# Kernel tuning notes

Measured on AMD Instinct MI355X. Metric: run time of the kernel, lower is better.

Reference implementation:

```python
import jax, jax.numpy as jnp
import numpy as np

HIDDEN = 1024   # config.hidden_dim
FF = 4096       # expert MLP hidden (4*hidden)
E = 8           # config.num_experts
K = 2           # config.num_selected_experts (top_k)


def setup_inputs() -> dict:
    key = jax.random.key(0)
    ks = jax.random.split(key, 5)
    s = 0.02
    x = jax.random.normal(ks[0], (2, 2048, HIDDEN), jnp.float32)
    Wr = jax.random.normal(ks[1], (HIDDEN, E), jnp.float32) * s   # router (no bias)
    W1 = jax.random.normal(ks[2], (E, HIDDEN, FF), jnp.float32) * s
    b1 = jnp.zeros((E, FF), jnp.float32)
    W2 = jax.random.normal(ks[3], (E, FF, HIDDEN), jnp.float32) * s
    b2 = jnp.zeros((E, HIDDEN), jnp.float32)
    return {"x": x, "Wr": Wr, "W1": W1, "b1": b1, "W2": W2, "b2": b2}


def reference(x, Wr, W1, b1, W2, b2):
    xs = x.reshape(-1, x.shape[-1])            # [T, H]
    router_logits = xs @ Wr                    # [T, E]
    # softmax_order == 'softmax_topk': softmax over all experts in fp32, then top-k
    all_probs = jax.nn.softmax(router_logits.astype(jnp.float32), axis=-1)
    weights, selected_experts = jax.lax.top_k(all_probs, K)   # [T, K], [T, K]
    T = xs.shape[0]
    # per-token per-expert combine weight (zero where expert not selected)
    combine = jnp.zeros((T, E), jnp.float32).at[
        jnp.arange(T)[:, None], selected_experts
    ].add(weights)                              # [T, E]
    out = jnp.zeros_like(xs)
    for e in range(E):                          # fixed small loop over experts
        h = jax.nn.gelu(xs @ W1[e] + b1[e])     # [T, FF]
        y = h @ W2[e] + b2[e]                   # [T, H]
        out = out + combine[:, e, None].astype(xs.dtype) * y
    return out.reshape(x.shape), router_logits, selected_experts
```

## Files before the change

kernel.cpp:

```cpp
#include <hip/hip_runtime.h>
#include <hip/hip_bf16.h>
#include <stdint.h>

#define HID 1024
#define FFD 4096
#define FFH 2048
#define NE  8
#define NTOK 4096
#define BM 128
#define BN 128
#define BK 32
#define RBCAP 72
#define ROWCAP (RBCAP*BM)

typedef __attribute__((ext_vector_type(8))) short short8;
typedef __attribute__((ext_vector_type(4))) float f32x4;

__device__ __forceinline__ unsigned short f2bf(float f){
  union { float f; unsigned u; } v; v.f = f;
  return (unsigned short)((v.u + 0x7FFFu + ((v.u >> 16) & 1u)) >> 16);
}

__device__ __forceinline__ float gelu_f(float x){
  float u = 0.7978845608028654f * (x + 0.044715f * x * x * x);
  return 0.5f * x * (1.0f + tanhf(u));
}

__device__ __forceinline__ void gload_lds16(const void* g, void* l){
  __builtin_amdgcn_global_load_lds((const __attribute__((address_space(1))) void*)g,
                                   (__attribute__((address_space(3))) void*)l,
                                   16, 0, 0);
}

__global__ __launch_bounds__(256) void router_k(
    const float* __restrict__ x, const float* __restrict__ Wr,
    float* __restrict__ out_logits, float* __restrict__ out_sel,
    int* __restrict__ tok_sel, float* __restrict__ tok_w)
{
  const int lane = threadIdx.x & 63;
  const int t = (blockIdx.x << 2) + (threadIdx.x >> 6);
  const float* xr = x + (size_t)t * HID;
  double acc[NE];
  #pragma unroll
  for (int e = 0; e < NE; ++e) acc[e] = 0.0;
  #pragma unroll
  for (int i = 0; i < 4; ++i) {
    const int h0 = i * 256 + lane * 4;
    float4 xv = *(const float4*)(xr + h0);
    #pragma unroll
    for (int r = 0; r < 4; ++r) {
      float xs = (&xv.x)[r];
      float4 w0 = *(const float4*)(Wr + (size_t)(h0 + r) * NE);
      float4 w1 = *(const float4*)(Wr + (size_t)(h0 + r) * NE + 4);
      acc[0] += (double)xs * w0.x;  acc[1] += (double)xs * w0.y;
      acc[2] += (double)xs * w0.z;  acc[3] += (double)xs * w0.w;
      acc[4] += (double)xs * w1.x;  acc[5] += (double)xs * w1.y;
      acc[6] += (double)xs * w1.z;  acc[7] += (double)xs * w1.w;
    }
  }
  #pragma unroll
  for (int off = 32; off > 0; off >>= 1) {
    #pragma unroll
    for (int e = 0; e < NE; ++e) acc[e] += __shfl_down(acc[e], off);
  }
  if (lane == 0) {
    float lg[NE], p[NE];
    float mx = -3.4e38f;
    #pragma unroll
    for (int e = 0; e < NE; ++e) { lg[e] = (float)acc[e]; mx = fmaxf(mx, lg[e]); }
    float s = 0.f;
    #pragma unroll
    for (int e = 0; e < NE; ++e) { p[e] = expf(lg[e] - mx); s += p[e]; }
    float inv = 1.0f / s;
    #pragma unroll
    for (int e = 0; e < NE; ++e) p[e] *= inv;
    #pragma unroll
    for (int e = 0; e < NE; ++e) out_logits[(size_t)t * NE + e] = lg[e];
    int e0 = 0;
    #pragma unroll
    for (int e = 1; e < NE; ++e) if (p[e] > p[e0]) e0 = e;
    int e1 = (e0 == 0) ? 1 : 0;
    #pragma unroll
    for (int e = 0; e < NE; ++e) if (e != e0 && p[e] > p[e1]) e1 = e;
    out_sel[(size_t)t * 2 + 0] = (float)e0;
    out_sel[(size_t)t * 2 + 1] = (float)e1;
    tok_sel[t * 2 + 0] = e0;  tok_sel[t * 2 + 1] = e1;
    tok_w[t * 2 + 0] = p[e0]; tok_w[t * 2 + 1] = p[e1];
  }
}

__global__ __launch_bounds__(1024) void part_k(
    const int* __restrict__ tok_sel, const float* __restrict__ tok_w,
    int* __restrict__ pair_tok, float* __restrict__ pair_w,
    int* __restrict__ rb2e, int* __restrict__ rb2row, int* __restrict__ nrb)
{
  __shared__ unsigned sc[1024][NE];
  __shared__ unsigned shOffs[NE];
  const int tid = threadIdx.x;
  int pe[8];
  unsigned cnt[NE] = {0,0,0,0,0,0,0,0};
  #pragma unroll
  for (int j = 0; j < 8; ++j) {
    int e = tok_sel[tid * 8 + j];
    pe[j] = e;
    #pragma unroll
    for (int k = 0; k < NE; ++k) cnt[k] += (e == k) ? 1u : 0u;
  }
  #pragma unroll
  for (int k = 0; k < NE; ++k) sc[tid][k] = cnt[k];
  __syncthreads();
  for (int off = 1; off < 1024; off <<= 1) {
    unsigned v[NE];
    const bool act = (tid >= off);
    if (act) {
      #pragma unroll
      for (int k = 0; k < NE; ++k) v[k] = sc[tid - off][k];
    }
    __syncthreads();
    if (act) {
      #pragma unroll
      for (int k = 0; k < NE; ++k) sc[tid][k] += v[k];
    }
    __syncthreads();
  }
  if (tid == 0) {
    unsigned row = 0; int rb = 0;
    #pragma unroll
    for (int e = 0; e < NE; ++e) {
      shOffs[e] = row;
      int nb = (int)((sc[1023][e] + 127u) >> 7);
      for (int b = 0; b < nb; ++b) { rb2e[rb] = e; rb2row[rb] = (int)row + b * BM; ++rb; }
      row += (unsigned)nb << 7;
    }
    nrb[0] = rb;
  }
  __syncthreads();
  #pragma unroll
  for (int j = 0; j < 8; ++j) {
    int e = pe[j];
    int rank = 0;
    #pragma unroll
    for (int j2 = 0; j2 < 8; ++j2) if (j2 < j) rank += (pe[j2] == e) ? 1 : 0;
    unsigned prev = (tid > 0) ? sc[tid - 1][e] : 0u;
    int p = (int)(shOffs[e] + prev) + rank;
    int q = tid * 8 + j;
    pair_tok[p] = q >> 1;
    pair_w[p] = tok_w[q];
  }
}

__global__ __launch_bounds__(256) void gather_k(
    const float* __restrict__ x, const int* __restrict__ pair_tok, unsigned short* __restrict__ Xg)
{
  const int lane = threadIdx.x & 63;
  const int p = (blockIdx.x << 2) + (threadIdx.x >> 6);
  int t = pair_tok[p];
  if (t < 0) return;
  const float* src = x + (size_t)t * HID;
  unsigned short* dst = Xg + (size_t)p * HID;
  #pragma unroll
  for (int i = 0; i < 4; ++i) {
    float4 v = *(const float4*)(src + lane * 4 + i * 256);
    unsigned a = (unsigned)f2bf(v.x) | ((unsigned)f2bf(v.y) << 16);
    unsigned b = (unsigned)f2bf(v.z) | ((unsigned)f2bf(v.w) << 16);
    *(uint2*)(dst + lane * 4 + i * 256) = make_uint2(a, b);
  }
}

template<int KSUB, int NSUB>
__global__ __launch_bounds__(256) void wtrans_k(const float* __restrict__ in,
                                               unsigned short* __restrict__ out,
                                               int ld_in, size_t in_estride)
{
  const int tilesN = NSUB / 64;
  const int tk = blockIdx.x / tilesN, tn = blockIdx.x % tilesN;
  const int k0 = tk * 64, n0 = tn * 64;
  const float* ine = in + (size_t)blockIdx.y * in_estride;
  unsigned short* oute = out + (size_t)blockIdx.y * KSUB * NSUB;
  __shared__ unsigned short lds[64][65];
  const int t = threadIdx.x;
  #pragma unroll
  for (int i = 0; i < 4; ++i) {
    int f = i * 256 + t;
    int krow = f >> 4, c4 = (f & 15) * 4;
    float4 v = *(const float4*)(ine + (size_t)(k0 + krow) * ld_in + n0 + c4);
    lds[c4 + 0][krow] = f2bf(v.x);
    lds[c4 + 1][krow] = f2bf(v.y);
    lds[c4 + 2][krow] = f2bf(v.z);
    lds[c4 + 3][krow] = f2bf(v.w);
  }
  __syncthreads();
  #pragma unroll
  for (int i = 0; i < 4; ++i) {
    int g = i * 256 + t;
    int nrow = g >> 4, kc = (g & 15) * 4;
    unsigned short a0 = lds[nrow][kc], a1 = lds[nrow][kc + 1];
    unsigned short a2 = lds[nrow][kc + 2], a3 = lds[nrow][kc + 3];
    uint2 w;
    w.x = (unsigned)a0 | ((unsigned)a1 << 16);
    w.y = (unsigned)a2 | ((unsigned)a3 << 16);
    *(uint2*)(oute + (size_t)(n0 + nrow) * KSUB + k0 + kc) = w;
  }
}

template<int KDIM, int NDIM, int BIAS_STRIDE, bool DOGELU, bool ADD_BIAS>
__global__ __launch_bounds__(256) void gemm_k(
    const unsigned short* __restrict__ A, const unsigned short* __restrict__ Bt,
    const float* __restrict__ bias,
    const int* __restrict__ nrb, const int* __restrict__ rb2e, const int* __restrict__ rb2row,
    unsigned short* __restrict__ Hout,
    const int* __restrict__ pair_tok, const float* __restrict__ pair_w,
    float* __restrict__ out)
{
  if ((int)blockIdx.y >= nrb[0]) return;
  const int e    = rb2e[blockIdx.y];
  const int row0 = rb2row[blockIdx.y];
  const int bn   = blockIdx.x * BN;

  __shared__ __align__(16) unsigned short As[BM * BK];
  __shared__ __align__(16) unsigned short Bs[BN * BK];

  const int tid = threadIdx.x;
  const int lane = tid & 63, wave = tid >> 6;
  const int wm = wave >> 1, wn = wave & 1;
  const unsigned short* Be = Bt + (size_t)e * KDIM * NDIM;

  f32x4 acc[4][4];
  #pragma unroll
  for (int m = 0; m < 4; ++m)
    #pragma unroll
    for (int n = 0; n < 4; ++n) acc[m][n] = f32x4{0.f, 0.f, 0.f, 0.f};

  for (int kt = 0; kt < KDIM; kt += BK) {
    #pragma unroll
    for (int r = 0; r < 2; ++r) {
      int c = r * 256 + tid;
      int mrow = c >> 2;
      int koff = (c & 3) * 8;
      const void* gpa = (const void*)(A + (size_t)(row0 + mrow) * KDIM + kt + koff);
      void* lpa = (void*)(As + (size_t)(r * 256 + wave * 64) * 8);
      gload_lds16(gpa, lpa);
      const void* gpb = (const void*)(Be + (size_t)(bn + mrow) * KDIM + kt + koff);
      void* lpb = (void*)(Bs + (size_t)(r * 256 + wave * 64) * 8);
      gload_lds16(gpb, lpb);
    }
    __syncthreads();

    const int kc = lane >> 4, rsel0 = lane & 15;
    short8 af[4], bfr[4];
    #pragma unroll
    for (int m = 0; m < 4; ++m)
      af[m] = *(const short8*)&As[(wm * 64 + m * 16 + rsel0) * BK + kc * 8];
    #pragma unroll
    for (int n = 0; n < 4; ++n)
      bfr[n] = *(const short8*)&Bs[(wn * 64 + n * 16 + rsel0) * BK + kc * 8];
    #pragma unroll
    for (int m = 0; m < 4; ++m)
      #pragma unroll
      for (int n = 0; n < 4; ++n)
        acc[m][n] = __builtin_amdgcn_mfma_f32_16x16x32_bf16(af[m], bfr[n], acc[m][n], 0, 0, 0);

    __syncthreads();
  }

  const int rsel = lane & 15, quad = lane >> 4;
  float bvv[4];
  #pragma unroll
  for (int n = 0; n < 4; ++n)
    bvv[n] = ADD_BIAS ? bias[(size_t)e * BIAS_STRIDE + bn + wn * 64 + n * 16 + rsel] : 0.f;

  if constexpr (DOGELU) {
    #pragma unroll
    for (int m = 0; m < 4; ++m) {
      int r0 = row0 + wm * 64 + m * 16 + quad * 4;
      #pragma unroll
      for (int n = 0; n < 4; ++n) {
        int col = bn + wn * 64 + n * 16 + rsel;
        unsigned short* hp = Hout + (size_t)r0 * NDIM + col;
        #pragma unroll
        for (int i = 0; i < 4; ++i) {
          float v = acc[m][n][i] + bvv[n];
          hp[(size_t)i * NDIM] = f2bf(gelu_f(v));
        }
      }
    }
  } else {
    #pragma unroll
    for (int m = 0; m < 4; ++m) {
      #pragma unroll
      for (int i = 0; i < 4; ++i) {
        int p = row0 + wm * 64 + m * 16 + quad * 4 + i;
        int t = pair_tok[p];
        if (t < 0) continue;
        float w = pair_w[p];
        float* op = out + (size_t)t * HID;
        #pragma unroll
        for (int n = 0; n < 4; ++n) {
          int col = bn + wn * 64 + n * 16 + rsel;
          atomicAdd(op + col, w * (acc[m][n][i] + bvv[n]));
        }
      }
    }
  }
}

extern "C" void kernel_launch(void* const* d_in, const int* in_sizes, int n_in,
                              void* d_out, int out_size, void* d_ws, size_t ws_size,
                              hipStream_t stream)
{
  const float* x  = (const float*)d_in[0];
  const float* Wr = (const float*)d_in[1];
  const float* W1 = (const float*)d_in[2];
  const float* b1 = (const float*)d_in[3];
  const float* W2 = (const float*)d_in[4];
  const float* b2 = (const float*)d_in[5];

  float* out        = (float*)d_out;
  float* out_logits = out + (size_t)NTOK * HID;
  float* out_sel    = out_logits + (size_t)NTOK * NE;

  char* ws = (char*)d_ws;
  int*   nrb      = (int*)(ws + 128);
  int*   rb2e     = (int*)(ws + 256);
  int*   rb2row   = (int*)(ws + 768);
  int*   tok_sel  = (int*)(ws + 1280);
  float* tok_w    = (float*)(ws + 34048);
  int*   pair_tok = (int*)(ws + 66816);
  float* pair_w   = (float*)(ws + 103680);
  unsigned short* Xg  = (unsigned short*)(ws + 140800);
  unsigned short* Hh  = (unsigned short*)(ws + 19015168);
  unsigned short* Wth = (unsigned short*)(ws + 56763904);

  hipMemsetAsync(pair_tok, 0xFF, (size_t)ROWCAP * 4, stream);
  hipMemsetAsync(d_out, 0, (size_t)out_size * 4, stream);

  router_k<<<NTOK / 4, 256, 0, stream>>>(x, Wr, out_logits, out_sel, tok_sel, tok_w);
  part_k<<<1, 1024, 0, stream>>>(tok_sel, tok_w, pair_tok, pair_w, rb2e, rb2row, nrb);
  gather_k<<<ROWCAP / 4, 256, 0, stream>>>(x, pair_tok, Xg);

  for (int h = 0; h < 2; ++h) {
    dim3 gt1((HID / 64) * (FFH / 64), NE);
    wtrans_k<HID, FFH><<<gt1, 256, 0, stream>>>(
        W1 + (size_t)h * FFH, Wth, FFD, (size_t)HID * FFD);
    dim3 g1(FFH / BN, RBCAP);
    gemm_k<HID, FFH, FFD, true, true><<<g1, 256, 0, stream>>>(
        Xg, Wth, b1 + (size_t)h * FFH, nrb, rb2e, rb2row, Hh, nullptr, nullptr, nullptr);
    dim3 gt2((FFH / 64) * (HID / 64), NE);
    wtrans_k<FFH, HID><<<gt2, 256, 0, stream>>>(
        W2 + (size_t)h * FFH * HID, Wth, HID, (size_t)FFD * HID);
    if (h == 0)
      gemm_k<FFH, HID, HID, false, true><<<dim3(HID / BN, RBCAP), 256, 0, stream>>>(
          Hh, Wth, b2, nrb, rb2e, rb2row, nullptr, pair_tok, pair_w, out);
    else
      gemm_k<FFH, HID, HID, false, false><<<dim3(HID / BN, RBCAP), 256, 0, stream>>>(
          Hh, Wth, b2, nrb, rb2e, rb2row, nullptr, pair_tok, pair_w, out);
  }
}
```

Baseline: 662.2 us.

## Double-buffer GEMM LDS tiles, swizzle block order, widen weight-transpose tiles

The grouped GEMM now uses two LDS buffers so the next K-tile's global-to-LDS load is issued before the MFMAs on the current tile, removing one barrier per iteration. It also flattens the grid to 1D with an XCD-style swizzle of block ids, aiming for better L2 locality across the chiplets. The weight transpose kernel handles 128x64 tiles and writes with 16-byte vector stores instead of 8-byte ones. LDS use doubles in the GEMM, which may reduce occupancy.

```diff
diff --git a/kernel.cpp b/kernel.cpp
--- a/kernel.cpp
+++ b/kernel.cpp
@@ -174,36 +174,40 @@
 {
   const int tilesN = NSUB / 64;
   const int tk = blockIdx.x / tilesN, tn = blockIdx.x % tilesN;
-  const int k0 = tk * 64, n0 = tn * 64;
+  const int k0 = tk * 128, n0 = tn * 64;
   const float* ine = in + (size_t)blockIdx.y * in_estride;
-  unsigned short* oute = out + (size_t)blockIdx.y * KSUB * NSUB;
-  __shared__ unsigned short lds[64][65];
+  unsigned short* oute = out + (size_t)blockIdx.y * ((size_t)KSUB * NSUB);
+  __shared__ unsigned short lds[64][136];
   const int t = threadIdx.x;
   #pragma unroll
+  for (int i = 0; i < 2; ++i) {
+    int idx = i * 256 + t;
+    int c4  = (idx & 15) * 4;
+    int kr4 = (idx >> 4) * 4;
+    float4 v[4];
+    #pragma unroll
+    for (int jj = 0; jj < 4; ++jj)
+      v[jj] = *(const float4*)(ine + (size_t)(k0 + kr4 + jj) * ld_in + n0 + c4);
+    #pragma unroll
+    for (int j = 0; j < 4; ++j) {
+      uint2 w;
+      w.x = (unsigned)f2bf((&v[0].x)[j]) | ((unsigned)f2bf((&v[1].x)[j]) << 16);
+      w.y = (unsigned)f2bf((&v[2].x)[j]) | ((unsigned)f2bf((&v[3].x)[j]) << 16);
+      *(uint2*)&lds[c4 + j][kr4] = w;
+    }
+  }
+  __syncthreads();
+  #pragma unroll
   for (int i = 0; i < 4; ++i) {
-    int f = i * 256 + t;
-    int krow = f >> 4, c4 = (f & 15) * 4;
-    float4 v = *(const float4*)(ine + (size_t)(k0 + krow) * ld_in + n0 + c4);
-    lds[c4 + 0][krow] = f2bf(v.x);
-    lds[c4 + 1][krow] = f2bf(v.y);
-    lds[c4 + 2][krow] = f2bf(v.z);
-    lds[c4 + 3][krow] = f2bf(v.w);
-  }
-  __syncthreads();
-  #pragma unroll
-  for (int i = 0; i < 4; ++i) {
-    int g = i * 256 + t;
-    int nrow = g >> 4, kc = (g & 15) * 4;
-    unsigned short a0 = lds[nrow][kc], a1 = lds[nrow][kc + 1];
-    unsigned short a2 = lds[nrow][kc + 2], a3 = lds[nrow][kc + 3];
-    uint2 w;
-    w.x = (unsigned)a0 | ((unsigned)a1 << 16);
-    w.y = (unsigned)a2 | ((unsigned)a3 << 16);
-    *(uint2*)(oute + (size_t)(n0 + nrow) * KSUB + k0 + kc) = w;
-  }
-}
-
-template<int KDIM, int NDIM, int BIAS_STRIDE, bool DOGELU, bool ADD_BIAS>
+    int idx = i * 256 + t;
+    int nrow = idx >> 4;
+    int kc8  = (idx & 15) * 8;
+    uint4 w = *(const uint4*)&lds[nrow][kc8];
+    *(uint4*)(oute + (size_t)(n0 + nrow) * KSUB + k0 + kc8) = w;
+  }
+}
+
+template<int KDIM, int NDIM, int XT, int BIAS_STRIDE, bool DOGELU, bool ADD_BIAS>
 __global__ __launch_bounds__(256) void gemm_k(
     const unsigned short* __restrict__ A, const unsigned short* __restrict__ Bt,
     const float* __restrict__ bias,
@@ -212,13 +216,18 @@
     const int* __restrict__ pair_tok, const float* __restrict__ pair_w,
     float* __restrict__ out)
 {
-  if ((int)blockIdx.y >= nrb[0]) return;
-  const int e    = rb2e[blockIdx.y];
-  const int row0 = rb2row[blockIdx.y];
-  const int bn   = blockIdx.x * BN;
-
-  __shared__ __align__(16) unsigned short As[BM * BK];
-  __shared__ __align__(16) unsigned short Bs[BN * BK];
+  const int nwg = XT * RBCAP;
+  const int bid = (int)blockIdx.x;
+  const int swz = (bid & 7) * (nwg >> 3) + (bid >> 3);
+  const int bx  = swz % XT;
+  const int by  = swz / XT;
+  if (by >= nrb[0]) return;
+  const int e    = rb2e[by];
+  const int row0 = rb2row[by];
+  const int bn   = bx * BN;
+
+  __shared__ __align__(16) unsigned short As[2][BM * BK];
+  __shared__ __align__(16) unsigned short Bs[2][BN * BK];
 
   const int tid = threadIdx.x;
   const int lane = tid & 63, wave = tid >> 6;
@@ -231,35 +240,43 @@
     #pragma unroll
     for (int n = 0; n < 4; ++n) acc[m][n] = f32x4{0.f, 0.f, 0.f, 0.f};
 
-  for (int kt = 0; kt < KDIM; kt += BK) {
+  const int mrow0 = tid >> 2;
+  const int koff0 = (tid & 3) * 8;
+  const int ldsoff = wave * 64 * 8;
+
+  auto stage = [&](int buf, int kt) {
     #pragma unroll
     for (int r = 0; r < 2; ++r) {
-      int c = r * 256 + tid;
-      int mrow = c >> 2;
-      int koff = (c & 3) * 8;
-      const void* gpa = (const void*)(A + (size_t)(row0 + mrow) * KDIM + kt + koff);
-      void* lpa = (void*)(As + (size_t)(r * 256 + wave * 64) * 8);
-      gload_lds16(gpa, lpa);
-      const void* gpb = (const void*)(Be + (size_t)(bn + mrow) * KDIM + kt + koff);
-      void* lpb = (void*)(Bs + (size_t)(r * 256 + wave * 64) * 8);
-      gload_lds16(gpb, lpb);
-    }
-    __syncthreads();
-
-    const int kc = lane >> 4, rsel0 = lane & 15;
+      int mrow = mrow0 + r * 64;
+      gload_lds16((const void*)(A + (size_t)(row0 + mrow) * KDIM + kt + koff0),
+                  (void*)(&As[buf][0] + (size_t)(r * 256 * 8) + ldsoff));
+      gload_lds16((const void*)(Be + (size_t)(bn + mrow) * KDIM + kt + koff0),
+                  (void*)(&Bs[buf][0] + (size_t)(r * 256 * 8) + ldsoff));
+    }
+  };
+
+  constexpr int NIT = KDIM / BK;
+  stage(0, 0);
+  __syncthreads();
+
+  const int kc = lane >> 4, rsel0 = lane & 15;
+  for (int it = 0; it < NIT; ++it) {
+    const int cur = it & 1;
+    if (it + 1 < NIT) stage(cur ^ 1, (it + 1) * BK);
+    const unsigned short* Ac = &As[cur][0];
+    const unsigned short* Bc = &Bs[cur][0];
     short8 af[4], bfr[4];
     #pragma unroll
     for (int m = 0; m < 4; ++m)
-      af[m] = *(const short8*)&As[(wm * 64 + m * 16 + rsel0) * BK + kc * 8];
+      af[m] = *(const short8*)&Ac[(wm * 64 + m * 16 + rsel0) * BK + kc * 8];
     #pragma unroll
     for (int n = 0; n < 4; ++n)
-      bfr[n] = *(const short8*)&Bs[(wn * 64 + n * 16 + rsel0) * BK + kc * 8];
+      bfr[n] = *(const short8*)&Bc[(wn * 64 + n * 16 + rsel0) * BK + kc * 8];
     #pragma unroll
     for (int m = 0; m < 4; ++m)
       #pragma unroll
       for (int n = 0; n < 4; ++n)
         acc[m][n] = __builtin_amdgcn_mfma_f32_16x16x32_bf16(af[m], bfr[n], acc[m][n], 0, 0, 0);
-
     __syncthreads();
   }
 
@@ -339,20 +356,19 @@
   gather_k<<<ROWCAP / 4, 256, 0, stream>>>(x, pair_tok, Xg);
 
   for (int h = 0; h < 2; ++h) {
-    dim3 gt1((HID / 64) * (FFH / 64), NE);
+    dim3 gt1((HID / 128) * (FFH / 64), NE);
     wtrans_k<HID, FFH><<<gt1, 256, 0, stream>>>(
         W1 + (size_t)h * FFH, Wth, FFD, (size_t)HID * FFD);
-    dim3 g1(FFH / BN, RBCAP);
-    gemm_k<HID, FFH, FFD, true, true><<<g1, 256, 0, stream>>>(
+    gemm_k<HID, FFH, FFH / BN, FFD, true, true><<<(FFH / BN) * RBCAP, 256, 0, stream>>>(
         Xg, Wth, b1 + (size_t)h * FFH, nrb, rb2e, rb2row, Hh, nullptr, nullptr, nullptr);
-    dim3 gt2((FFH / 64) * (HID / 64), NE);
+    dim3 gt2((FFH / 128) * (HID / 64), NE);
     wtrans_k<FFH, HID><<<gt2, 256, 0, stream>>>(
         W2 + (size_t)h * FFH * HID, Wth, HID, (size_t)FFD * HID);
     if (h == 0)
-      gemm_k<FFH, HID, HID, false, true><<<dim3(HID / BN, RBCAP), 256, 0, stream>>>(
+      gemm_k<FFH, HID, HID / BN, HID, false, true><<<(HID / BN) * RBCAP, 256, 0, stream>>>(
           Hh, Wth, b2, nrb, rb2e, rb2row, nullptr, pair_tok, pair_w, out);
     else
-      gemm_k<FFH, HID, HID, false, false><<<dim3(HID / BN, RBCAP), 256, 0, stream>>>(
+      gemm_k<FFH, HID, HID / BN, HID, false, false><<<(HID / BN) * RBCAP, 256, 0, stream>>>(
           Hh, Wth, b2, nrb, rb2e, rb2row, nullptr, pair_tok, pair_w, out);
   }
 }
```

Result: no change. 672.7 us (+1.6%).
